# Kernel tuning notes

Measured on AMD Instinct MI355X. Metric: run time of the kernel, lower is better.

The kernel has to match this reference:

```python
import jax, jax.numpy as jnp
import numpy as np

N, D, H = 4096, 1024, 4096
EPS = 1e-5


def setup_inputs() -> dict:
    key = jax.random.key(0)
    ks = jax.random.split(key, 12)
    s_in = 1.0 / np.sqrt(D)
    s_hid = 1.0 / np.sqrt(H)
    return {
        "x": jax.random.normal(ks[0], (N, D), dtype=jnp.float32),
        "Wq": jax.random.uniform(ks[1], (D, H), jnp.float32, -s_in, s_in),
        "Wk": jax.random.uniform(ks[2], (D, H), jnp.float32, -s_in, s_in),
        "Wv": jax.random.uniform(ks[3], (D, H), jnp.float32, -s_in, s_in),
        "Wo": jax.random.uniform(ks[4], (H, D), jnp.float32, -s_hid, s_hid),
        "W1": jax.random.uniform(ks[5], (D, H), jnp.float32, -s_in, s_in),
        "b1": jax.random.uniform(ks[6], (H,), jnp.float32, -s_in, s_in),
        "W2": jax.random.uniform(ks[7], (H, D), jnp.float32, -s_hid, s_hid),
        "b2": jax.random.uniform(ks[8], (D,), jnp.float32, -s_hid, s_hid),
        "g1": jnp.ones((D,), jnp.float32),
        "be1": jnp.zeros((D,), jnp.float32),
        "g2": jnp.ones((D,), jnp.float32),
        "be2": jnp.zeros((D,), jnp.float32),
    }


def _layernorm(x, g, b):
    mu = jnp.mean(x, axis=-1, keepdims=True)
    var = jnp.mean(jnp.square(x - mu), axis=-1, keepdims=True)
    return (x - mu) * jax.lax.rsqrt(var + EPS) * g + b


def reference(x, Wq, Wk, Wv, Wo, W1, b1, W2, b2, g1, be1, g2, be2):
    # --- attention (single head, unscaled, as in the source) ---
    q = x @ Wq                      # [N, H]
    k = x @ Wk                      # [N, H]
    v = x @ Wv                      # [N, H]
    scores = jax.nn.softmax(q @ k.T, axis=-1)  # [N, N]
    attn = (scores @ v) @ Wo        # [N, D]
    h = _layernorm(x + attn, g1, be1)
    # --- feed-forward ---
    ff = jax.nn.relu(h @ W1 + b1) @ W2 + b2
    return _layernorm(h + ff, g2, be2)
```

## Files before the change

### kernel.cpp

```cpp
#include <hip/hip_runtime.h>
#include <hip/hip_bf16.h>

using f16 = _Float16;
typedef __attribute__((ext_vector_type(8))) f16 half8;
typedef __attribute__((ext_vector_type(4))) f16 half4;
typedef __attribute__((ext_vector_type(4))) float floatx4;

#define LN_EPS 1e-5f

__device__ __forceinline__ void gload_lds16(const f16* g, f16* l) {
  __builtin_amdgcn_global_load_lds(
      (const __attribute__((address_space(1))) void*)g,
      (__attribute__((address_space(3))) void*)l, 16, 0, 0);
}

#define CFENCE asm volatile("" ::: "memory")
#define WAIT_VM(N) asm volatile("s_waitcnt vmcnt(" #N ")" ::: "memory")
#define WAIT_LGKM0                                     \
  do {                                                 \
    asm volatile("s_waitcnt lgkmcnt(0)" ::: "memory"); \
    __builtin_amdgcn_sched_barrier(0);                 \
  } while (0)
#define BARRIER()                    \
  do {                               \
    CFENCE;                          \
    __builtin_amdgcn_s_barrier();    \
    CFENCE;                          \
  } while (0)

template <int EPI>
__device__ __forceinline__ void gemm256_core(
    const f16* __restrict__ A, const f16* __restrict__ B,
    f16* __restrict__ Cz, const float* __restrict__ bias,
    int lda, int ldb, int ldc, int kper, int kbeg, int bm, int bn,
    f16* smp, float* __restrict__ Smax, float* __restrict__ Ssum) {
  const int t = threadIdx.x;
  const int wave = t >> 6, lane = t & 63;
  const int wm = (wave >> 2) << 7;
  const int wn = (wave & 3) << 6;
  const int lrow = lane & 15, lkc = lane >> 4;

  const int srow = lane >> 3;
  const int schunk = ((lane & 7) ^ srow) << 3;
  const f16* Ag = A + (size_t)(bm + wave * 16 + srow) * lda + kbeg + schunk;
  const f16* Bg = B + (size_t)(bn + wave * 16 + srow) * ldb + kbeg + schunk;

  const int co0 = ((lkc ^ (lrow & 7)) << 3);
  const int co1 = (((4 + lkc) ^ (lrow & 7)) << 3);

  floatx4 acc[8][4] = {};
  half8 af[4][2];
  half8 bf[2][2][2];

  auto STAGE = [&](int b, int tt, int h) {
    if (h < 2) {
      const f16* src = Ag + (size_t)(h * 128) * lda + tt * 64;
      f16* d = smp + (b * 2) * 16384 + h * 8192 + wave * 1024;
      gload_lds16(src, d);
      gload_lds16(src + (size_t)8 * lda, d + 512);
    } else {
      const f16* src = Bg + (size_t)((h - 2) * 128) * ldb + tt * 64;
      f16* d = smp + (b * 2 + 1) * 16384 + (h - 2) * 8192 + wave * 1024;
      gload_lds16(src, d);
      gload_lds16(src + (size_t)8 * ldb, d + 512);
    }
  };
  auto LDA = [&](int b, int qm) {
    const f16* base = smp + (b * 2) * 16384 + (wm + qm * 64 + lrow) * 64;
#pragma unroll
    for (int fm = 0; fm < 4; ++fm) {
      af[fm][0] = *(const half8*)(base + fm * (16 * 64) + co0);
      af[fm][1] = *(const half8*)(base + fm * (16 * 64) + co1);
    }
  };
  auto LDB = [&](int b, int qn) {
    const f16* base = smp + (b * 2 + 1) * 16384 + (wn + qn * 32 + lrow) * 64;
#pragma unroll
    for (int fn = 0; fn < 2; ++fn) {
      bf[qn][fn][0] = *(const half8*)(base + fn * (16 * 64) + co0);
      bf[qn][fn][1] = *(const half8*)(base + fn * (16 * 64) + co1);
    }
  };
  auto MFMAQ = [&](int qm, int qn) {
    __builtin_amdgcn_s_setprio(1);
#pragma unroll
    for (int kk = 0; kk < 2; ++kk)
#pragma unroll
      for (int fm = 0; fm < 4; ++fm)
#pragma unroll
        for (int fn = 0; fn < 2; ++fn)
          acc[qm * 4 + fm][qn * 2 + fn] =
              __builtin_amdgcn_mfma_f32_16x16x32_f16(
                  af[fm][kk], bf[qn][fn][kk], acc[qm * 4 + fm][qn * 2 + fn],
                  0, 0, 0);
    __builtin_amdgcn_s_setprio(0);
  };

  const int NT = kper >> 6;
  const int NI = NT >> 1;

  STAGE(0, 0, 0); STAGE(0, 0, 1); STAGE(0, 0, 2); STAGE(0, 0, 3);
  STAGE(1, 1, 0);
  WAIT_VM(2);
  BARRIER();

  for (int i = 0; i < NI; ++i) {
    const bool last = (i == NI - 1);
    const int tb = 2 * i;
    LDA(0, 0); LDB(0, 0); STAGE(1, tb + 1, 1);
    BARRIER(); MFMAQ(0, 0); BARRIER();
    LDB(0, 1); STAGE(1, tb + 1, 2);
    BARRIER(); MFMAQ(0, 1); BARRIER();
    LDA(0, 1); STAGE(1, tb + 1, 3);
    BARRIER(); MFMAQ(1, 0); BARRIER();
    if (!last) {
      STAGE(0, tb + 2, 0);
      WAIT_VM(2);
    } else {
      WAIT_VM(0);
    }
    BARRIER(); MFMAQ(1, 1); BARRIER();
    LDA(1, 0); LDB(1, 0);
    if (!last) STAGE(0, tb + 2, 1);
    BARRIER(); MFMAQ(0, 0); BARRIER();
    LDB(1, 1);
    if (!last) STAGE(0, tb + 2, 2);
    BARRIER(); MFMAQ(0, 1); BARRIER();
    LDA(1, 1);
    if (!last) STAGE(0, tb + 2, 3);
    BARRIER(); MFMAQ(1, 0); BARRIER();
    if (!last) {
      STAGE(1, tb + 3, 0);
      WAIT_VM(2);
    }
    BARRIER(); MFMAQ(1, 1); BARRIER();
  }

  const int crow0 = bm + wm + lkc * 4;
  const int ccol0 = bn + wn + lrow;
#pragma unroll
  for (int i = 0; i < 8; ++i) {
#pragma unroll
    for (int r2 = 0; r2 < 4; ++r2) {
      const size_t row = (size_t)(crow0 + i * 16 + r2);
#pragma unroll
      for (int j = 0; j < 4; ++j) {
        const int col = ccol0 + j * 16;
        float v = acc[i][j][r2];
        if (EPI == 2) v = fmaxf(v + bias[col], 0.0f);
        Cz[row * (size_t)ldc + col] = (f16)v;
      }
    }
  }
  if (EPI == 3) {
    const int chunk = (bn + wn) >> 6;
#pragma unroll
    for (int i = 0; i < 8; ++i) {
#pragma unroll
      for (int r2 = 0; r2 < 4; ++r2) {
        float mx = fmaxf(fmaxf(acc[i][0][r2], acc[i][1][r2]),
                         fmaxf(acc[i][2][r2], acc[i][3][r2]));
#pragma unroll
        for (int m_ = 8; m_ >= 1; m_ >>= 1) mx = fmaxf(mx, __shfl_xor(mx, m_));
        float s = 0.0f;
#pragma unroll
        for (int j = 0; j < 4; ++j) s += __expf(acc[i][j][r2] - mx);
#pragma unroll
        for (int m_ = 8; m_ >= 1; m_ >>= 1) s += __shfl_xor(s, m_);
        if (lrow == 0) {
          const int row = crow0 + i * 16 + r2;
          Smax[(size_t)row * 64 + chunk] = mx;
          Ssum[(size_t)row * 64 + chunk] = s;
        }
      }
    }
  }
}

__device__ __forceinline__ int xcd_swizzle(int id, int nwg) {
  const int q = nwg >> 3, r = nwg & 7;
  const int xcd = id & 7, lin = id >> 3;
  return (xcd < r ? xcd * (q + 1) : r * (q + 1) + (xcd - r) * q) + lin;
}

template <int EPI>
__global__ __launch_bounds__(512, 2) void gemm_nt256(
    const f16* __restrict__ A, const f16* __restrict__ B,
    f16* __restrict__ Ch, const float* __restrict__ bias,
    float* __restrict__ Smax, float* __restrict__ Ssum,
    int M, int Nc, int K, int lda, int ldb, int ldc) {
  __shared__ f16 sm[4][256 * 64];
  const int gx = gridDim.x, gy = gridDim.y;
  const int nwg = gx * gy * gridDim.z;
  const int id = blockIdx.x + gx * (blockIdx.y + gy * blockIdx.z);
  const int nid = xcd_swizzle(id, nwg);
  const int bx = nid % gx;
  const int by = (nid / gx) % gy;
  const int bz = nid / (gx * gy);
  const int kper = K / gridDim.z;
  gemm256_core<EPI>(A, B, Ch + (size_t)bz * M * ldc, bias, lda, ldb, ldc,
                    kper, bz * kper, by << 8, bx << 8, &sm[0][0], Smax, Ssum);
}

__global__ __launch_bounds__(512, 2) void gemm_pre256(
    const f16* __restrict__ Wkb, const f16* __restrict__ Wqb,
    const f16* __restrict__ WoT, const f16* __restrict__ Wvb,
    f16* __restrict__ parQK, f16* __restrict__ parVO, int D, int H) {
  __shared__ f16 sm[4][256 * 64];
  const int id = blockIdx.x + 4 * (blockIdx.y + 4 * blockIdx.z);
  const int nid = xcd_swizzle(id, 256);
  const int bx = nid & 3, by = (nid >> 2) & 3, z = nid >> 4;
  const int zz = z & 7;
  const f16* A = (z < 8) ? Wkb : WoT;
  const f16* B = (z < 8) ? Wqb : Wvb;
  f16* slab = ((z < 8) ? parQK : parVO) + (size_t)zz * D * D;
  gemm256_core<1>(A, B, slab, nullptr, H, H, D, H / 8, zz * (H / 8),
                  by << 8, bx << 8, &sm[0][0], nullptr, nullptr);
}

__global__ __launch_bounds__(512, 2) void gemm_dual256(
    const f16* __restrict__ xb, const f16* __restrict__ WqkT,
    const f16* __restrict__ WvoT, f16* __restrict__ th,
    f16* __restrict__ xvoT, int N, int D) {
  __shared__ f16 sm[4][256 * 64];
  const int id = blockIdx.x + 4 * blockIdx.y;
  const int nid = xcd_swizzle(id, 128);
  const int bx = nid & 3, y = nid >> 2;
  if (y < 16)
    gemm256_core<1>(xb, WqkT, th, nullptr, D, D, D, D, 0,
                    y << 8, bx << 8, &sm[0][0], nullptr, nullptr);
  else
    gemm256_core<1>(WvoT, xb, xvoT, nullptr, D, D, N, D, 0,
                    bx << 8, (y - 16) << 8, &sm[0][0], nullptr, nullptr);
}

__global__ __launch_bounds__(512, 2) void gemm_pv256(
    const f16* __restrict__ A, const f16* __restrict__ B,
    f16* __restrict__ Ch, const float2* __restrict__ rowstat,
    int M, int Nc, int K, int lda, int ldb, int ldc) {
  __shared__ f16 sm[4][256 * 64];
  f16* smp = &sm[0][0];
  const int gx = gridDim.x, gy = gridDim.y;
  const int nwg = gx * gy * gridDim.z;
  const int id = blockIdx.x + gx * (blockIdx.y + gy * blockIdx.z);
  const int nid = xcd_swizzle(id, nwg);
  const int bx = nid % gx;
  const int by = (nid / gx) % gy;
  const int bz = nid / (gx * gy);
  const int kper = K / gridDim.z;
  const int kbeg = bz * kper;
  f16* Cz = Ch + (size_t)bz * M * ldc;
  const int bm = by << 8, bn = bx << 8;

  const int t = threadIdx.x;
  const int wave = t >> 6, lane = t & 63;
  const int wm = (wave >> 2) << 7;
  const int wn = (wave & 3) << 6;
  const int lrow = lane & 15, lkc = lane >> 4;
  const int srow = lane >> 3;
  const int schunk = ((lane & 7) ^ srow) << 3;
  const f16* Ag = A + (size_t)(bm + wave * 16 + srow) * lda + kbeg + schunk;
  const f16* Bg = B + (size_t)(bn + wave * 16 + srow) * ldb + kbeg + schunk;
  const int co0 = ((lkc ^ (lrow & 7)) << 3);
  const int co1 = (((4 + lkc) ^ (lrow & 7)) << 3);

  const int r0s = bm + wave * 16 + srow;
  const float2 st00 = rowstat[r0s], st01 = rowstat[r0s + 8];
  const float2 st10 = rowstat[r0s + 128], st11 = rowstat[r0s + 136];

  floatx4 acc[8][4] = {};
  half8 af[4][2];
  half8 bf[2][2][2];
  half8 pCa, pCb, p0a, p0b, p1a, p1b;

  auto ALOAD = [&](int tt, int h, half8& ra, half8& rb) {
    const f16* src = Ag + (size_t)(h * 128) * lda + tt * 64;
    ra = *(const half8*)(src);
    rb = *(const half8*)(src + (size_t)8 * lda);
  };
  auto AWRITE = [&](int b, int h, const half8& ra, const half8& rb,
                    const float2& sa, const float2& sb) {
    f16* d = smp + (b * 2) * 16384 + h * 8192 + wave * 1024 + lane * 8;
    half8 oa, ob;
#pragma unroll
    for (int k = 0; k < 8; ++k) {
      oa[k] = (f16)(__expf((float)ra[k] - sa.x) * sa.y);
      ob[k] = (f16)(__expf((float)rb[k] - sb.x) * sb.y);
    }
    *(half8*)d = oa;
    *(half8*)(d + 512) = ob;
  };
  auto BSTAGE = [&](int b, int tt, int h) {
    const f16* src = Bg + (size_t)((h - 2) * 128) * ldb + tt * 64;
    f16* d = smp + (b * 2 + 1) * 16384 + (h - 2) * 8192 + wave * 1024;
    gload_lds16(src, d);
    gload_lds16(src + (size_t)8 * ldb, d + 512);
  };
  auto LDA = [&](int b, int qm) {
    const f16* base = smp + (b * 2) * 16384 + (wm + qm * 64 + lrow) * 64;
#pragma unroll
    for (int fm = 0; fm < 4; ++fm) {
      af[fm][0] = *(const half8*)(base + fm * (16 * 64) + co0);
      af[fm][1] = *(const half8*)(base + fm * (16 * 64) + co1);
    }
  };
  auto LDB = [&](int b, int qn) {
    const f16* base = smp + (b * 2 + 1) * 16384 + (wn + qn * 32 + lrow) * 64;
#pragma unroll
    for (int fn = 0; fn < 2; ++fn) {
      bf[qn][fn][0] = *(const half8*)(base + fn * (16 * 64) + co0);
      bf[qn][fn][1] = *(const half8*)(base + fn * (16 * 64) + co1);
    }
  };
  auto MFMAQ = [&](int qm, int qn) {
    __builtin_amdgcn_s_setprio(1);
#pragma unroll
    for (int kk = 0; kk < 2; ++kk)
#pragma unroll
      for (int fm = 0; fm < 4; ++fm)
#pragma unroll
        for (int fn = 0; fn < 2; ++fn)
          acc[qm * 4 + fm][qn * 2 + fn] =
              __builtin_amdgcn_mfma_f32_16x16x32_f16(
                  af[fm][kk], bf[qn][fn][kk], acc[qm * 4 + fm][qn * 2 + fn],
                  0, 0, 0);
    __builtin_amdgcn_s_setprio(0);
  };

  const int NT = kper >> 6;
  const int NI = NT >> 1;

  ALOAD(0, 0, pCa, pCb);
  ALOAD(0, 1, p1a, p1b);
  BSTAGE(0, 0, 2); BSTAGE(0, 0, 3);
  ALOAD(1, 0, p0a, p0b);
  WAIT_VM(2);
  AWRITE(0, 0, pCa, pCb, st00, st01);
  AWRITE(0, 1, p1a, p1b, st10, st11);
  WAIT_LGKM0;
  BARRIER();

  for (int i = 0; i < NI; ++i) {
    const bool last = (i == NI - 1);
    const int tb = 2 * i;
    LDA(0, 0); LDB(0, 0); ALOAD(tb + 1, 1, p1a, p1b);
    BARRIER(); MFMAQ(0, 0); BARRIER();
    LDB(0, 1); BSTAGE(1, tb + 1, 2);
    BARRIER(); MFMAQ(0, 1); BARRIER();
    LDA(0, 1); BSTAGE(1, tb + 1, 3);
    BARRIER(); MFMAQ(1, 0); BARRIER();
    if (!last) {
      ALOAD(tb + 2, 0, pCa, pCb);
      WAIT_VM(2);
    } else {
      WAIT_VM(0);
    }
    AWRITE(1, 0, p0a, p0b, st00, st01);
    AWRITE(1, 1, p1a, p1b, st10, st11);
    WAIT_LGKM0;
    BARRIER(); MFMAQ(1, 1); BARRIER();
    LDA(1, 0); LDB(1, 0);
    if (!last) ALOAD(tb + 2, 1, p1a, p1b);
    BARRIER(); MFMAQ(0, 0); BARRIER();
    LDB(1, 1);
    if (!last) BSTAGE(0, tb + 2, 2);
    BARRIER(); MFMAQ(0, 1); BARRIER();
    LDA(1, 1);
    if (!last) BSTAGE(0, tb + 2, 3);
    BARRIER(); MFMAQ(1, 0); BARRIER();
    if (!last) {
      ALOAD(tb + 3, 0, p0a, p0b);
      WAIT_VM(2);
      AWRITE(0, 0, pCa, pCb, st00, st01);
      AWRITE(0, 1, p1a, p1b, st10, st11);
      WAIT_LGKM0;
    }
    BARRIER(); MFMAQ(1, 1); BARRIER();
  }

  const int crow0 = bm + wm + lkc * 4;
  const int ccol0 = bn + wn + lrow;
#pragma unroll
  for (int i = 0; i < 8; ++i) {
#pragma unroll
    for (int r2 = 0; r2 < 4; ++r2) {
      const size_t row = (size_t)(crow0 + i * 16 + r2);
#pragma unroll
      for (int j = 0; j < 4; ++j)
        Cz[row * (size_t)ldc + ccol0 + j * 16] = (f16)acc[i][j][r2];
    }
  }
}

__global__ void smax_reduce(const float* __restrict__ Smax,
                            const float* __restrict__ Ssum,
                            float2* __restrict__ rowstat) {
  const int row = blockIdx.x * 4 + (threadIdx.x >> 6);
  const int c = threadIdx.x & 63;
  const float mp = Smax[(size_t)row * 64 + c];
  const float sp = Ssum[(size_t)row * 64 + c];
  float m = mp;
#pragma unroll
  for (int off = 32; off > 0; off >>= 1) m = fmaxf(m, __shfl_xor(m, off));
  float s = sp * __expf(mp - m);
#pragma unroll
  for (int off = 32; off > 0; off >>= 1) s += __shfl_xor(s, off);
  if (c == 0) rowstat[row] = make_float2(m, 1.0f / s);
}

__global__ void prep_inputs(const float* x, const float* Wq, const float* Wk,
                            const float* Wv, const float* W1, const float* Wo,
                            const float* W2, f16* xb, f16* Wqb, f16* Wkb,
                            f16* Wvb, f16* W1T, f16* WoT, f16* W2T) {
  const int z = blockIdx.y;
  const int b = blockIdx.x;
  const int t = threadIdx.x;
  if (z >= 3) {
    const float* in = (z == 3) ? x : (z == 4) ? Wq : (z == 5) ? Wk : Wv;
    f16* out = (z == 3) ? xb : (z == 4) ? Wqb : (z == 5) ? Wkb : Wvb;
    const size_t i = ((size_t)b * 256 + t) * 16;
    const float4 a0 = *(const float4*)(in + i);
    const float4 a1 = *(const float4*)(in + i + 4);
    const float4 a2 = *(const float4*)(in + i + 8);
    const float4 a3 = *(const float4*)(in + i + 12);
    half8 v0 = {(f16)a0.x, (f16)a0.y, (f16)a0.z, (f16)a0.w,
                (f16)a1.x, (f16)a1.y, (f16)a1.z, (f16)a1.w};
    half8 v1 = {(f16)a2.x, (f16)a2.y, (f16)a2.z, (f16)a2.w,
                (f16)a3.x, (f16)a3.y, (f16)a3.z, (f16)a3.w};
    *(half8*)(out + i) = v0;
    *(half8*)(out + i + 8) = v1;
    return;
  }
  int R, C, tx, ty;
  const float* in;
  f16* out;
  if (z == 0) {
    R = 1024; C = 4096; in = W1; out = W1T;
    tx = b & 63; ty = b >> 6;
  } else {
    R = 4096; C = 1024; in = (z == 1) ? Wo : W2;
    out = (z == 1) ? WoT : W2T;
    tx = b & 15; ty = b >> 4;
  }
  const int r0 = ty << 6, c0 = tx << 6;
  __shared__ f16 lt[64 * 64];
  const int lr = t >> 4;
  const int lc = t & 15;
  const int q3 = lr & 3;
  const int rb = lr & ~3;
  const int myc = lc * 4 + q3;
#pragma unroll
  for (int rr = 0; rr < 4; ++rr) {
    const int r = lr + rr * 16;
    const float4 f = *(const float4*)(in + (size_t)(r0 + r) * C + c0 + lc * 4);
    float v0 = f.x, v1 = f.y, v2 = f.z, v3 = f.w;
    {
      const bool hi = (q3 & 2) != 0;
      float sA = hi ? v0 : v2;
      float sB = hi ? v1 : v3;
      sA = __shfl_xor(sA, 32);
      sB = __shfl_xor(sB, 32);
      if (hi) { v0 = sA; v1 = sB; } else { v2 = sA; v3 = sB; }
    }
    {
      const bool od = (q3 & 1) != 0;
      float sC = od ? v0 : v1;
      float sD = od ? v2 : v3;
      sC = __shfl_xor(sC, 16);
      sD = __shfl_xor(sD, 16);
      if (od) { v0 = sC; v2 = sD; } else { v1 = sC; v3 = sD; }
    }
    half4 hv = {(f16)v0, (f16)v1, (f16)v2, (f16)v3};
    const int rbase = rb + rr * 16;
    *(half4*)(lt + myc * 64 + (rbase ^ ((myc & 15) << 2))) = hv;
  }
  __syncthreads();
  const int oc = t >> 3, orr = (t & 7) << 3;
#pragma unroll
  for (int cc = 0; cc < 2; ++cc) {
    const int c = oc + cc * 32;
    const int swz = (c & 15) << 2;
    const half4 ha = *(const half4*)(lt + c * 64 + (orr ^ swz));
    const half4 hb4 = *(const half4*)(lt + c * 64 + ((orr + 4) ^ swz));
    half8 v = {ha[0], ha[1], ha[2], ha[3], hb4[0], hb4[1], hb4[2], hb4[3]};
    *(half8*)(out + (size_t)(c0 + c) * R + r0 + orr) = v;
  }
}

__global__ void reduce_dual(const f16* __restrict__ parQK,
                            const f16* __restrict__ parVO,
                            f16* __restrict__ WqkT, f16* __restrict__ WvoT,
                            int n) {
  const int half = gridDim.x >> 1;
  const bool second = blockIdx.x >= half;
  const f16* par = second ? parVO : parQK;
  f16* out = second ? WvoT : WqkT;
  const int b = second ? blockIdx.x - half : blockIdx.x;
  const int i = (b * 256 + threadIdx.x) * 8;
  float s[8] = {};
#pragma unroll
  for (int z = 0; z < 8; ++z) {
    const half8 p = *(const half8*)(par + (size_t)z * n + i);
#pragma unroll
    for (int k = 0; k < 8; ++k) s[k] += (float)p[k];
  }
  half8 o = {(f16)s[0], (f16)s[1], (f16)s[2], (f16)s[3],
             (f16)s[4], (f16)s[5], (f16)s[6], (f16)s[7]};
  *(half8*)(out + i) = o;
}

__global__ void add_ln(const float* __restrict__ a, const f16* __restrict__ b,
                       int nchunks, size_t cs, const float* __restrict__ bias,
                       const float* __restrict__ g, const float* __restrict__ be,
                       float* __restrict__ outf, f16* __restrict__ outh, int D) {
  const int row = blockIdx.x;
  const int t = threadIdx.x;
  const int lane = t & 63, wave = t >> 6;
  const float4 av = *(const float4*)(a + (size_t)row * D + t * 4);
  float s[4] = {av.x, av.y, av.z, av.w};
  for (int c = 0; c < nchunks; ++c) {
    const half4 bv = *(const half4*)(b + c * cs + (size_t)row * D + t * 4);
    s[0] += (float)bv[0]; s[1] += (float)bv[1];
    s[2] += (float)bv[2]; s[3] += (float)bv[3];
  }
  if (bias != nullptr) {
    const float4 bb = *(const float4*)(bias + t * 4);
    s[0] += bb.x; s[1] += bb.y; s[2] += bb.z; s[3] += bb.w;
  }
  float sum = s[0] + s[1] + s[2] + s[3];
  float sq = s[0] * s[0] + s[1] * s[1] + s[2] * s[2] + s[3] * s[3];
#pragma unroll
  for (int off = 32; off > 0; off >>= 1) {
    sum += __shfl_xor(sum, off);
    sq += __shfl_xor(sq, off);
  }
  __shared__ float red[8];
  if (lane == 0) {
    red[wave] = sum;
    red[4 + wave] = sq;
  }
  __syncthreads();
  sum = red[0] + red[1] + red[2] + red[3];
  sq = red[4] + red[5] + red[6] + red[7];
  const float mu = sum / (float)D;
  const float rv = rsqrtf(sq / (float)D - mu * mu + LN_EPS);
  const float4 gv = *(const float4*)(g + t * 4);
  const float4 bev = *(const float4*)(be + t * 4);
  float y0 = (s[0] - mu) * rv * gv.x + bev.x;
  float y1 = (s[1] - mu) * rv * gv.y + bev.y;
  float y2 = (s[2] - mu) * rv * gv.z + bev.z;
  float y3 = (s[3] - mu) * rv * gv.w + bev.w;
  if (outf != nullptr) {
    float4 o = {y0, y1, y2, y3};
    *(float4*)(outf + (size_t)row * D + t * 4) = o;
  }
  if (outh != nullptr) {
    f16* ob = outh + (size_t)row * D + t * 4;
    ob[0] = (f16)y0;
    ob[1] = (f16)y1;
    ob[2] = (f16)y2;
    ob[3] = (f16)y3;
  }
}

extern "C" void kernel_launch(void* const* d_in, const int* in_sizes, int n_in,
                              void* d_out, int out_size, void* d_ws,
                              size_t ws_size, hipStream_t stream) {
  constexpr int N = 4096, D = 1024, H = 4096;
  const float* x = (const float*)d_in[0];
  const float* Wq = (const float*)d_in[1];
  const float* Wk = (const float*)d_in[2];
  const float* Wv = (const float*)d_in[3];
  const float* Wo = (const float*)d_in[4];
  const float* W1 = (const float*)d_in[5];
  const float* b1 = (const float*)d_in[6];
  const float* W2 = (const float*)d_in[7];
  const float* b2 = (const float*)d_in[8];
  const float* g1 = (const float*)d_in[9];
  const float* be1 = (const float*)d_in[10];
  const float* g2 = (const float*)d_in[11];
  const float* be2 = (const float*)d_in[12];
  float* out = (float*)d_out;

  const size_t MB = 1024ull * 1024ull;
  char* w = (char*)d_ws;
  f16* xb   = (f16*)(w + 0 * MB);
  f16* Wqb  = (f16*)(w + 8 * MB);
  f16* Wkb  = (f16*)(w + 16 * MB);
  f16* Wvb  = (f16*)(w + 24 * MB);
  f16* WoT  = (f16*)(w + 32 * MB);
  f16* W1T  = (f16*)(w + 40 * MB);
  f16* W2T  = (f16*)(w + 48 * MB);
  f16* WqkT = (f16*)(w + 56 * MB);
  f16* WvoT = (f16*)(w + 58 * MB);
  f16* th   = (f16*)(w + 60 * MB);
  f16* xvoT = (f16*)(w + 68 * MB);
  f16* F1   = (f16*)(w + 76 * MB);
  f16* Sh   = (f16*)(w + 108 * MB);
  f16* parA = (f16*)(w + 140 * MB);
  float* hf = (float*)(w + 172 * MB);
  f16* hb   = (f16*)(w + 188 * MB);
  f16* parQK = (f16*)(w + 196 * MB);
  f16* parVO = (f16*)(w + 212 * MB);
  float* Smax = (float*)(w + 196 * MB);
  float* Ssum = (float*)(w + 197 * MB);
  float2* rowstat = (float2*)(w + 198 * MB);

  prep_inputs<<<dim3(1024, 7), 256, 0, stream>>>(
      x, Wq, Wk, Wv, W1, Wo, W2, xb, Wqb, Wkb, Wvb, W1T, WoT, W2T);

  gemm_pre256<<<dim3(4, 4, 16), 512, 0, stream>>>(
      Wkb, Wqb, WoT, Wvb, parQK, parVO, D, H);
  reduce_dual<<<2 * (D * D) / 2048, 256, 0, stream>>>(parQK, parVO, WqkT,
                                                      WvoT, D * D);

  gemm_dual256<<<dim3(4, 32), 512, 0, stream>>>(xb, WqkT, WvoT, th, xvoT,
                                                N, D);
  gemm_nt256<3><<<dim3(N / 256, N / 256, 1), 512, 0, stream>>>(
      th, xb, Sh, nullptr, Smax, Ssum, N, N, D, D, D, N);
  smax_reduce<<<N / 4, 256, 0, stream>>>(Smax, Ssum, rowstat);
  gemm_pv256<<<dim3(D / 256, N / 256, 4), 512, 0, stream>>>(
      Sh, xvoT, parA, rowstat, N, D, N, N, N, D);
  add_ln<<<N, 256, 0, stream>>>(x, parA, 4, (size_t)N * D, nullptr, g1, be1,
                                hf, hb, D);

  gemm_nt256<2><<<dim3(H / 256, N / 256, 1), 512, 0, stream>>>(
      hb, W1T, F1, b1, nullptr, nullptr, N, H, D, D, D, H);
  gemm_nt256<1><<<dim3(D / 256, N / 256, 4), 512, 0, stream>>>(
      F1, W2T, parA, nullptr, nullptr, nullptr, N, D, H, H, H, D);
  add_ln<<<N, 256, 0, stream>>>(hf, parA, 4, (size_t)N * D, b2, g2, be2,
                                out, nullptr, D);
}
```

Baseline: 491.0 us.

## Move softmax exponent into QK epilogue and rescale accumulators in PV GEMM

The QK^T GEMM epilogue now reduces the row max across the 256-wide tile through LDS and writes exp(s - tile_max) instead of raw scores. The PV GEMM therefore loads its A operand straight into LDS with async global_load_lds, dropping the register exp/scale path. Per-tile correction factors (exp of max differences and 1/sum) are computed by a new reduce kernel and applied as online-softmax style rescaling of the accumulators every four k-tiles and at the end. This cuts exp work and register staging in the PV loop, at the cost of an extra LDS reduction and two syncs in the QK epilogue.

```diff
diff --git a/kernel.cpp b/kernel.cpp
--- a/kernel.cpp
+++ b/kernel.cpp
@@ -16,11 +16,6 @@
 
 #define CFENCE asm volatile("" ::: "memory")
 #define WAIT_VM(N) asm volatile("s_waitcnt vmcnt(" #N ")" ::: "memory")
-#define WAIT_LGKM0                                     \
-  do {                                                 \
-    asm volatile("s_waitcnt lgkmcnt(0)" ::: "memory"); \
-    __builtin_amdgcn_sched_barrier(0);                 \
-  } while (0)
 #define BARRIER()                    \
   do {                               \
     CFENCE;                          \
@@ -138,39 +133,84 @@
 
   const int crow0 = bm + wm + lkc * 4;
   const int ccol0 = bn + wn + lrow;
-#pragma unroll
-  for (int i = 0; i < 8; ++i) {
-#pragma unroll
-    for (int r2 = 0; r2 < 4; ++r2) {
-      const size_t row = (size_t)(crow0 + i * 16 + r2);
-#pragma unroll
-      for (int j = 0; j < 4; ++j) {
-        const int col = ccol0 + j * 16;
-        float v = acc[i][j][r2];
-        if (EPI == 2) v = fmaxf(v + bias[col], 0.0f);
-        Cz[row * (size_t)ldc + col] = (f16)v;
-      }
-    }
-  }
   if (EPI == 3) {
-    const int chunk = (bn + wn) >> 6;
-#pragma unroll
-    for (int i = 0; i < 8; ++i) {
+    float* mt = (float*)smp;
+    float* st = ((float*)smp) + 1024;
+    const int wm2 = wave >> 2, wvc = wave & 3;
+    const int rb_ = lkc * 4;
+    float m256[8][4];
+#pragma unroll
+    for (int i = 0; i < 8; ++i)
 #pragma unroll
       for (int r2 = 0; r2 < 4; ++r2) {
         float mx = fmaxf(fmaxf(acc[i][0][r2], acc[i][1][r2]),
                          fmaxf(acc[i][2][r2], acc[i][3][r2]));
 #pragma unroll
-        for (int m_ = 8; m_ >= 1; m_ >>= 1) mx = fmaxf(mx, __shfl_xor(mx, m_));
+        for (int m_ = 8; m_ >= 1; m_ >>= 1)
+          mx = fmaxf(mx, __shfl_xor(mx, m_));
+        if (lrow == 0) mt[wave * 128 + rb_ + i * 16 + r2] = mx;
+      }
+    __syncthreads();
+#pragma unroll
+    for (int i = 0; i < 8; ++i)
+#pragma unroll
+      for (int r2 = 0; r2 < 4; ++r2) {
+        const int rl = rb_ + i * 16 + r2;
+        m256[i][r2] = fmaxf(
+            fmaxf(mt[(wm2 * 4 + 0) * 128 + rl], mt[(wm2 * 4 + 1) * 128 + rl]),
+            fmaxf(mt[(wm2 * 4 + 2) * 128 + rl], mt[(wm2 * 4 + 3) * 128 + rl]));
+      }
+#pragma unroll
+    for (int i = 0; i < 8; ++i)
+#pragma unroll
+      for (int r2 = 0; r2 < 4; ++r2) {
         float s = 0.0f;
 #pragma unroll
-        for (int j = 0; j < 4; ++j) s += __expf(acc[i][j][r2] - mx);
+        for (int j = 0; j < 4; ++j)
+          s += __expf(acc[i][j][r2] - m256[i][r2]);
 #pragma unroll
         for (int m_ = 8; m_ >= 1; m_ >>= 1) s += __shfl_xor(s, m_);
-        if (lrow == 0) {
+        if (lrow == 0) st[wave * 128 + rb_ + i * 16 + r2] = s;
+      }
+    __syncthreads();
+    if (wvc == 0 && lrow == 0) {
+      const int chunk = bn >> 8;
+#pragma unroll
+      for (int i = 0; i < 8; ++i)
+#pragma unroll
+        for (int r2 = 0; r2 < 4; ++r2) {
+          const int rl = rb_ + i * 16 + r2;
           const int row = crow0 + i * 16 + r2;
-          Smax[(size_t)row * 64 + chunk] = mx;
-          Ssum[(size_t)row * 64 + chunk] = s;
+          const float ss = st[(wm2 * 4 + 0) * 128 + rl] +
+                           st[(wm2 * 4 + 1) * 128 + rl] +
+                           st[(wm2 * 4 + 2) * 128 + rl] +
+                           st[(wm2 * 4 + 3) * 128 + rl];
+          Smax[(size_t)row * 16 + chunk] = m256[i][r2];
+          Ssum[(size_t)row * 16 + chunk] = ss;
+        }
+    }
+#pragma unroll
+    for (int i = 0; i < 8; ++i)
+#pragma unroll
+      for (int r2 = 0; r2 < 4; ++r2) {
+        const size_t row = (size_t)(crow0 + i * 16 + r2);
+#pragma unroll
+        for (int j = 0; j < 4; ++j)
+          Cz[row * (size_t)ldc + ccol0 + j * 16] =
+              (f16)__expf(acc[i][j][r2] - m256[i][r2]);
+      }
+  } else {
+#pragma unroll
+    for (int i = 0; i < 8; ++i) {
+#pragma unroll
+      for (int r2 = 0; r2 < 4; ++r2) {
+        const size_t row = (size_t)(crow0 + i * 16 + r2);
+#pragma unroll
+        for (int j = 0; j < 4; ++j) {
+          const int col = ccol0 + j * 16;
+          float v = acc[i][j][r2];
+          if (EPI == 2) v = fmaxf(v + bias[col], 0.0f);
+          Cz[row * (size_t)ldc + col] = (f16)v;
         }
       }
     }
@@ -236,9 +276,10 @@
 
 __global__ __launch_bounds__(512, 2) void gemm_pv256(
     const f16* __restrict__ A, const f16* __restrict__ B,
-    f16* __restrict__ Ch, const float2* __restrict__ rowstat,
+    f16* __restrict__ Ch, const float* __restrict__ Tfac,
     int M, int Nc, int K, int lda, int ldb, int ldc) {
   __shared__ f16 sm[4][256 * 64];
+  __shared__ float tf[256 * 4];
   f16* smp = &sm[0][0];
   const int gx = gridDim.x, gy = gridDim.y;
   const int nwg = gx * gy * gridDim.z;
@@ -264,37 +305,22 @@
   const int co0 = ((lkc ^ (lrow & 7)) << 3);
   const int co1 = (((4 + lkc) ^ (lrow & 7)) << 3);
 
-  const int r0s = bm + wave * 16 + srow;
-  const float2 st00 = rowstat[r0s], st01 = rowstat[r0s + 8];
-  const float2 st10 = rowstat[r0s + 128], st11 = rowstat[r0s + 136];
-
   floatx4 acc[8][4] = {};
   half8 af[4][2];
   half8 bf[2][2][2];
-  half8 pCa, pCb, p0a, p0b, p1a, p1b;
-
-  auto ALOAD = [&](int tt, int h, half8& ra, half8& rb) {
-    const f16* src = Ag + (size_t)(h * 128) * lda + tt * 64;
-    ra = *(const half8*)(src);
-    rb = *(const half8*)(src + (size_t)8 * lda);
-  };
-  auto AWRITE = [&](int b, int h, const half8& ra, const half8& rb,
-                    const float2& sa, const float2& sb) {
-    f16* d = smp + (b * 2) * 16384 + h * 8192 + wave * 1024 + lane * 8;
-    half8 oa, ob;
-#pragma unroll
-    for (int k = 0; k < 8; ++k) {
-      oa[k] = (f16)(__expf((float)ra[k] - sa.x) * sa.y);
-      ob[k] = (f16)(__expf((float)rb[k] - sb.x) * sb.y);
-    }
-    *(half8*)d = oa;
-    *(half8*)(d + 512) = ob;
-  };
-  auto BSTAGE = [&](int b, int tt, int h) {
-    const f16* src = Bg + (size_t)((h - 2) * 128) * ldb + tt * 64;
-    f16* d = smp + (b * 2 + 1) * 16384 + (h - 2) * 8192 + wave * 1024;
-    gload_lds16(src, d);
-    gload_lds16(src + (size_t)8 * ldb, d + 512);
+
+  auto STAGE = [&](int b, int tt, int h) {
+    if (h < 2) {
+      const f16* src = Ag + (size_t)(h * 128) * lda + tt * 64;
+      f16* d = smp + (b * 2) * 16384 + h * 8192 + wave * 1024;
+      gload_lds16(src, d);
+      gload_lds16(src + (size_t)8 * lda, d + 512);
+    } else {
+      const f16* src = Bg + (size_t)((h - 2) * 128) * ldb + tt * 64;
+      f16* d = smp + (b * 2 + 1) * 16384 + (h - 2) * 8192 + wave * 1024;
+      gload_lds16(src, d);
+      gload_lds16(src + (size_t)8 * ldb, d + 512);
+    }
   };
   auto LDA = [&](int b, int qm) {
     const f16* base = smp + (b * 2) * 16384 + (wm + qm * 64 + lrow) * 64;
@@ -327,53 +353,62 @@
     __builtin_amdgcn_s_setprio(0);
   };
 
+  {
+    const int r = t >> 1, p = (t & 1) * 2;
+    const float2 tv =
+        *(const float2*)(Tfac + (size_t)(bm + r) * 16 + bz * 4 + p);
+    tf[r * 4 + p] = tv.x;
+    tf[r * 4 + p + 1] = tv.y;
+    asm volatile("s_waitcnt lgkmcnt(0)" ::: "memory");
+  }
+
   const int NT = kper >> 6;
   const int NI = NT >> 1;
 
-  ALOAD(0, 0, pCa, pCb);
-  ALOAD(0, 1, p1a, p1b);
-  BSTAGE(0, 0, 2); BSTAGE(0, 0, 3);
-  ALOAD(1, 0, p0a, p0b);
+  STAGE(0, 0, 0); STAGE(0, 0, 1); STAGE(0, 0, 2); STAGE(0, 0, 3);
+  STAGE(1, 1, 0);
   WAIT_VM(2);
-  AWRITE(0, 0, pCa, pCb, st00, st01);
-  AWRITE(0, 1, p1a, p1b, st10, st11);
-  WAIT_LGKM0;
   BARRIER();
 
   for (int i = 0; i < NI; ++i) {
     const bool last = (i == NI - 1);
     const int tb = 2 * i;
-    LDA(0, 0); LDB(0, 0); ALOAD(tb + 1, 1, p1a, p1b);
+    LDA(0, 0); LDB(0, 0); STAGE(1, tb + 1, 1);
+    if (i > 0 && (i & 1) == 0) {
+      const int tix = i >> 1;
+#pragma unroll
+      for (int i16 = 0; i16 < 8; ++i16)
+#pragma unroll
+        for (int r2 = 0; r2 < 4; ++r2) {
+          const float f = tf[(wm + lkc * 4 + i16 * 16 + r2) * 4 + tix];
+#pragma unroll
+          for (int j = 0; j < 4; ++j) acc[i16][j][r2] *= f;
+        }
+    }
     BARRIER(); MFMAQ(0, 0); BARRIER();
-    LDB(0, 1); BSTAGE(1, tb + 1, 2);
+    LDB(0, 1); STAGE(1, tb + 1, 2);
     BARRIER(); MFMAQ(0, 1); BARRIER();
-    LDA(0, 1); BSTAGE(1, tb + 1, 3);
+    LDA(0, 1); STAGE(1, tb + 1, 3);
     BARRIER(); MFMAQ(1, 0); BARRIER();
     if (!last) {
-      ALOAD(tb + 2, 0, pCa, pCb);
+      STAGE(0, tb + 2, 0);
       WAIT_VM(2);
     } else {
       WAIT_VM(0);
     }
-    AWRITE(1, 0, p0a, p0b, st00, st01);
-    AWRITE(1, 1, p1a, p1b, st10, st11);
-    WAIT_LGKM0;
     BARRIER(); MFMAQ(1, 1); BARRIER();
     LDA(1, 0); LDB(1, 0);
-    if (!last) ALOAD(tb + 2, 1, p1a, p1b);
+    if (!last) STAGE(0, tb + 2, 1);
     BARRIER(); MFMAQ(0, 0); BARRIER();
     LDB(1, 1);
-    if (!last) BSTAGE(0, tb + 2, 2);
+    if (!last) STAGE(0, tb + 2, 2);
     BARRIER(); MFMAQ(0, 1); BARRIER();
     LDA(1, 1);
-    if (!last) BSTAGE(0, tb + 2, 3);
+    if (!last) STAGE(0, tb + 2, 3);
     BARRIER(); MFMAQ(1, 0); BARRIER();
     if (!last) {
-      ALOAD(tb + 3, 0, p0a, p0b);
+      STAGE(1, tb + 3, 0);
       WAIT_VM(2);
-      AWRITE(0, 0, pCa, pCb, st00, st01);
-      AWRITE(0, 1, p1a, p1b, st10, st11);
-      WAIT_LGKM0;
     }
     BARRIER(); MFMAQ(1, 1); BARRIER();
   }
@@ -384,28 +419,40 @@
   for (int i = 0; i < 8; ++i) {
 #pragma unroll
     for (int r2 = 0; r2 < 4; ++r2) {
+      const float f = tf[(wm + lkc * 4 + i * 16 + r2) * 4];
       const size_t row = (size_t)(crow0 + i * 16 + r2);
 #pragma unroll
       for (int j = 0; j < 4; ++j)
-        Cz[row * (size_t)ldc + ccol0 + j * 16] = (f16)acc[i][j][r2];
-    }
-  }
-}
-
-__global__ void smax_reduce(const float* __restrict__ Smax,
-                            const float* __restrict__ Ssum,
-                            float2* __restrict__ rowstat) {
-  const int row = blockIdx.x * 4 + (threadIdx.x >> 6);
-  const int c = threadIdx.x & 63;
-  const float mp = Smax[(size_t)row * 64 + c];
-  const float sp = Ssum[(size_t)row * 64 + c];
-  float m = mp;
-#pragma unroll
-  for (int off = 32; off > 0; off >>= 1) m = fmaxf(m, __shfl_xor(m, off));
-  float s = sp * __expf(mp - m);
-#pragma unroll
-  for (int off = 32; off > 0; off >>= 1) s += __shfl_xor(s, off);
-  if (c == 0) rowstat[row] = make_float2(m, 1.0f / s);
+        Cz[row * (size_t)ldc + ccol0 + j * 16] = (f16)(acc[i][j][r2] * f);
+    }
+  }
+}
+
+__global__ void smax_reduce2(const float* __restrict__ Smax,
+                             const float* __restrict__ Ssum,
+                             float* __restrict__ Tfac) {
+  const int t = threadIdx.x;
+  const int row = blockIdx.x * 16 + (t >> 4);
+  const int c = t & 15;
+  const int lane = t & 63;
+  const float mc = Smax[(size_t)row * 16 + c];
+  const float sc = Ssum[(size_t)row * 16 + c];
+  float m = mc;
+#pragma unroll
+  for (int off = 8; off >= 1; off >>= 1) m = fmaxf(m, __shfl_xor(m, off));
+  float s = sc * __expf(mc - m);
+#pragma unroll
+  for (int off = 8; off >= 1; off >>= 1) s += __shfl_xor(s, off);
+  const float inv = 1.0f / s;
+  const int base = lane & ~15;
+  const float mprev = __shfl(mc, base | ((c - 1) & 15));
+  const float mlast = __shfl(mc, base | (c | 3));
+  float f;
+  if ((c & 3) == 0)
+    f = __expf(mlast - m) * inv;
+  else
+    f = __expf(mprev - mc);
+  Tfac[(size_t)row * 16 + c] = f;
 }
 
 __global__ void prep_inputs(const float* x, const float* Wq, const float* Wk,
@@ -604,7 +651,7 @@
   f16* parVO = (f16*)(w + 212 * MB);
   float* Smax = (float*)(w + 196 * MB);
   float* Ssum = (float*)(w + 197 * MB);
-  float2* rowstat = (float2*)(w + 198 * MB);
+  float* Tfac = (float*)(w + 198 * MB);
 
   prep_inputs<<<dim3(1024, 7), 256, 0, stream>>>(
       x, Wq, Wk, Wv, W1, Wo, W2, xb, Wqb, Wkb, Wvb, W1T, WoT, W2T);
@@ -618,9 +665,9 @@
                                                 N, D);
   gemm_nt256<3><<<dim3(N / 256, N / 256, 1), 512, 0, stream>>>(
       th, xb, Sh, nullptr, Smax, Ssum, N, N, D, D, D, N);
-  smax_reduce<<<N / 4, 256, 0, stream>>>(Smax, Ssum, rowstat);
+  smax_reduce2<<<N / 16, 256, 0, stream>>>(Smax, Ssum, Tfac);
   gemm_pv256<<<dim3(D / 256, N / 256, 4), 512, 0, stream>>>(
-      Sh, xvoT, parA, rowstat, N, D, N, N, N, D);
+      Sh, xvoT, parA, Tfac, N, D, N, N, N, D);
   add_ln<<<N, 256, 0, stream>>>(x, parA, 4, (size_t)N * D, nullptr, g1, be1,
                                 hf, hb, D);
 
```

Measured after the change: 439.6 us. -10.5%, faster.
